# Kernel tuning notes

Hardware: AMD Instinct MI355X
Metric: run time of the kernel (lower is better)

The kernel has to match this reference:

```python
import jax, jax.numpy as jnp
import numpy as np

TOP_K = 2
EPS = 1e-6

def setup_inputs() -> dict:
    key = jax.random.key(0)
    ks = jax.random.split(key, 6)
    Bt, S, D, E, R = 4, 4096, 1024, 8, 4
    s = lambda d: 1.0 / np.sqrt(d)
    return {
        "x": jax.random.normal(ks[0], (Bt, S, D), jnp.float32),
        "W_base": jax.random.normal(ks[1], (D, D), jnp.float32) * s(D),
        "b_base": jax.random.normal(ks[2], (D,), jnp.float32) * 0.02,
        "W_router": jax.random.normal(ks[3], (E, D), jnp.float32) * s(D),
        "A": jax.random.normal(ks[4], (E, D, R), jnp.float32) * s(D),
        "B": jax.random.normal(ks[5], (E, R, D), jnp.float32) * s(R),
    }

def reference(x, W_base, b_base, W_router, A, B):
    # frozen base linear: [b,s,d] @ [out,d]^T + bias
    base_out = jnp.einsum('bsd,od->bso', x, W_base) + b_base
    # router softmax gate over experts
    logits = jnp.einsum('bsd,ed->bse', x, W_router)
    gate = jax.nn.softmax(logits, axis=-1)
    # top-k scatter-mask (values kept are the gate values themselves)
    topv, topi = jax.lax.top_k(gate, TOP_K)                    # [b,s,k]
    mask = jnp.sum(jax.nn.one_hot(topi, gate.shape[-1], dtype=gate.dtype), axis=-2)
    gate = gate * mask
    gate = gate / (jnp.sum(gate, axis=-1, keepdims=True) + EPS)
    # batched rank-4 LoRA experts, gating applied in low-rank space
    h = jnp.einsum('bsd,edr->bser', x, A)                      # [b,s,E,r]
    hg = h * gate[..., None]                                   # weight before up-proj
    lora_out = jnp.einsum('bser,ero->bso', hg, B)
    return base_out + lora_out
```

## Files before the change

kernel.cpp:

```cpp
#include <hip/hip_runtime.h>
#include <cstdint>

typedef __attribute__((ext_vector_type(8))) short short8;
typedef __attribute__((ext_vector_type(4))) float f32x4;

__device__ inline unsigned short f2bf(float f){
  union { float f; uint32_t u; } v; v.f = f;
  uint32_t r = v.u + 0x7FFFu + ((v.u >> 16) & 1u);
  return (unsigned short)(r >> 16);
}

#define GLL(gp, lp) __builtin_amdgcn_global_load_lds(              \
    (const __attribute__((address_space(1))) void*)(gp),           \
    (__attribute__((address_space(3))) void*)(lp), 16, 0, 0)

__global__ __launch_bounds__(256) void kconv(const float* __restrict__ W,
                                             const float* __restrict__ A,
                                             const float* __restrict__ Bm,
                                             unsigned short* __restrict__ Wb,
                                             unsigned short* __restrict__ BTt,
                                             unsigned short* __restrict__ W2b){
  int i = blockIdx.x * 256 + threadIdx.x;
  Wb[i] = f2bf(W[i]);
  if (i < 32768){
    int o = i >> 5, c = i & 31;
    BTt[i] = f2bf(Bm[(size_t)c*1024 + o]);
    int n = i >> 10, d = i & 1023;
    W2b[i] = f2bf(A[(((size_t)(n>>2))*1024 + d)*4 + (n&3)]);
  }
}

__global__ __launch_bounds__(256) void kxl(const float* __restrict__ x,
                                           const float* __restrict__ Wr,
                                           unsigned short* __restrict__ xb,
                                           float* __restrict__ gate){
  __shared__ float wr[8192];
  const int tid  = threadIdx.x;
  const int lane = tid & 63;
  const int w    = tid >> 6;
  {
    const float4* s  = (const float4*)Wr;
    float4*       d4 = (float4*)wr;
    #pragma unroll
    for (int j=0;j<8;j++) d4[j*256+tid] = s[j*256+tid];
  }
  __syncthreads();
  const float4* wr4 = (const float4*)wr;
  #pragma unroll 1
  for (int tt=0; tt<4; tt++){
    const size_t tok = (size_t)blockIdx.x*16 + w*4 + tt;
    const float4* xr = (const float4*)(x + tok*1024);
    ushort4*      xd = (ushort4*)(xb + tok*1024);
    float4 xv[4];
    #pragma unroll
    for (int c=0;c<4;c++){
      xv[c] = xr[c*64 + lane];
      ushort4 o4; o4.x=f2bf(xv[c].x); o4.y=f2bf(xv[c].y);
      o4.z=f2bf(xv[c].z); o4.w=f2bf(xv[c].w);
      xd[c*64 + lane] = o4;
    }
    float p[8];
    #pragma unroll
    for (int e=0;e<8;e++){
      float a = 0.f;
      #pragma unroll
      for (int c=0;c<4;c++){
        float4 wv = wr4[e*256 + c*64 + lane];
        a += xv[c].x*wv.x + xv[c].y*wv.y + xv[c].z*wv.z + xv[c].w*wv.w;
      }
      p[e] = a;
    }
    #pragma unroll
    for (int off=32; off; off>>=1){
      #pragma unroll
      for (int e=0;e<8;e++) p[e] += __shfl_xor(p[e], off, 64);
    }
    if (lane == 0){
      float mx = p[0];
      #pragma unroll
      for (int e=1;e<8;e++) mx = fmaxf(mx, p[e]);
      float ex[8], s2 = 0.f;
      #pragma unroll
      for (int e=0;e<8;e++){ ex[e] = __expf(p[e]-mx); s2 += ex[e]; }
      int i1 = 0; float v1 = ex[0];
      #pragma unroll
      for (int e=1;e<8;e++) if (ex[e] > v1){ v1 = ex[e]; i1 = e; }
      int i2 = -1; float v2 = -1.f;
      #pragma unroll
      for (int e=0;e<8;e++) if (e != i1 && ex[e] > v2){ v2 = ex[e]; i2 = e; }
      float g1 = v1/s2, g2 = v2/s2;
      float rs = 1.f/(g1 + g2 + 1e-6f);
      float* go = gate + tok*8;
      #pragma unroll
      for (int e=0;e<8;e++) go[e] = (e==i1 ? g1 : (e==i2 ? g2 : 0.f)) * rs;
    }
  }
}

__global__ __launch_bounds__(256) void kh(const unsigned short* __restrict__ xbp,
                                          const unsigned short* __restrict__ W2b,
                                          const float* __restrict__ gate,
                                          unsigned short* __restrict__ HG){
  const int tid  = threadIdx.x;
  const int lane = tid & 63;
  const int wid  = tid >> 6;
  const int lrow = lane & 15;
  const int lk   = (lane >> 4) * 8;
  const int tok0 = blockIdx.x*64 + wid*16;
  f32x4 acc0 = {0.f,0.f,0.f,0.f}, acc1 = {0.f,0.f,0.f,0.f};
  const unsigned short* b0 = W2b + (size_t)lrow*1024 + lk;
  const unsigned short* b1 = W2b + (size_t)(16+lrow)*1024 + lk;
  const unsigned short* ar = xbp + (size_t)(tok0+lrow)*1024 + lk;
  #pragma unroll 4
  for (int ks=0; ks<32; ks++){
    short8 av  = *(const short8*)(ar + ks*32);
    short8 bv0 = *(const short8*)(b0 + ks*32);
    short8 bv1 = *(const short8*)(b1 + ks*32);
    acc0 = __builtin_amdgcn_mfma_f32_16x16x32_bf16(av, bv0, acc0, 0, 0, 0);
    acc1 = __builtin_amdgcn_mfma_f32_16x16x32_bf16(av, bv1, acc1, 0, 0, 0);
  }
  #pragma unroll
  for (int j=0;j<4;j++){
    int tok = tok0 + (lane>>4)*4 + j;
    float g0 = gate[(size_t)tok*8 + (lrow>>2)];
    float g1 = gate[(size_t)tok*8 + 4 + (lrow>>2)];
    HG[(size_t)tok*32 + lrow]      = f2bf(acc0[j]*g0);
    HG[(size_t)tok*32 + 16 + lrow] = f2bf(acc1[j]*g1);
  }
}

__global__ __launch_bounds__(512, 2) void kgemm3(const unsigned short* __restrict__ xb,
                                                 const unsigned short* __restrict__ Wb,
                                                 const unsigned short* __restrict__ BTt,
                                                 const unsigned short* __restrict__ HG,
                                                 const float* __restrict__ bias,
                                                 float* __restrict__ out){
  __shared__ char lds[131072];
  char* ldsc = lds;
  const int tid  = threadIdx.x;
  const int lane = tid & 63;
  const int w    = tid >> 6;
  const int xcd  = blockIdx.x & 7, jj = blockIdx.x >> 3;
  const int nblk = xcd >> 1;
  const int mblk = (xcd & 1)*32 + jj;
  const int m0 = mblk << 8, n0 = nblk << 8;
  const int wm = w >> 2, wn = w & 3;
  const int lrow = lane & 15;
  const int q    = lane >> 4;

  const int swzk = (lrow & 7) << 4;
  int offA[8], offB[4];
  #pragma unroll
  for (int fm=0; fm<8; fm++){ int r = wm*128 + fm*16 + lrow; offA[fm] = r*128 + ((q<<4) ^ swzk); }
  #pragma unroll
  for (int fn=0; fn<4; fn++){ int r = wn*64  + fn*16 + lrow; offB[fn] = r*128 + ((q<<4) ^ swzk); }

  const int rowL = lane >> 3;
  const int colb = ((lane & 7) ^ rowL) << 4;
  const int rbA = (w>>2)*128 + (w&3)*16;
  const int rbB = w*16;
  const char* AgA = (const char*)xb + ((size_t)(m0 + rbA + rowL) << 11) + colb;
  const char* BgA = (const char*)Wb + ((size_t)(n0 + rbB + rowL) << 11) + colb;

#define STG_A(tt, h, ss) do{                                                        \
    GLL(AgA + (size_t)(h)*131072 + (tt)*128,                                        \
        ldsc + (ss)*32768 + (rbA + (h)*64)*128 + lane*16);                          \
    GLL(AgA + (size_t)(h)*131072 + 16384 + (tt)*128,                                \
        ldsc + (ss)*32768 + (rbA + (h)*64 + 8)*128 + lane*16); }while(0)
#define STG_B(tt, h, ss) do{                                                        \
    GLL(BgA + (size_t)(h)*262144 + (tt)*128,                                        \
        ldsc + 65536 + (ss)*32768 + (rbB + (h)*128)*128 + lane*16);                 \
    GLL(BgA + (size_t)(h)*262144 + 16384 + (tt)*128,                                \
        ldsc + 65536 + (ss)*32768 + (rbB + (h)*128 + 8)*128 + lane*16); }while(0)

  f32x4 acc[8][4];
  #pragma unroll
  for (int a=0;a<8;a++)
    #pragma unroll
    for (int b=0;b<4;b++) acc[a][b] = (f32x4){0.f,0.f,0.f,0.f};

  STG_A(0,0,0); STG_A(0,1,0); STG_B(0,0,0); STG_B(0,1,0);
  STG_A(1,0,1); STG_A(1,1,1);
  asm volatile("s_waitcnt vmcnt(4)" ::: "memory");
  __builtin_amdgcn_s_barrier();

  #pragma unroll 1
  for (int t = 0; t < 16; ++t){
    const int s = t & 1, sn = s ^ 1;
    const char* Ab = ldsc + s*32768;
    const char* Bb = ldsc + 65536 + s*32768;
    short8 a[8], b0[4], b1[4];
    #pragma unroll
    for (int fm=0; fm<4; fm++){
      a[fm*2]   = *(const short8*)(Ab + offA[fm]);
      a[fm*2+1] = *(const short8*)(Ab + (offA[fm]^64));
    }
    #pragma unroll
    for (int fn=0; fn<2; fn++){
      b0[fn*2]   = *(const short8*)(Bb + offB[fn]);
      b0[fn*2+1] = *(const short8*)(Bb + (offB[fn]^64));
    }
    if (t < 15) STG_B(t+1, 0, sn);
    __builtin_amdgcn_s_barrier();
    __builtin_amdgcn_s_setprio(1);
    #pragma unroll
    for (int kk=0;kk<2;kk++)
      #pragma unroll
      for (int fm=0;fm<4;fm++)
        #pragma unroll
        for (int fn=0;fn<2;fn++)
          acc[fm][fn] = __builtin_amdgcn_mfma_f32_16x16x32_bf16(a[fm*2+kk], b0[fn*2+kk], acc[fm][fn], 0, 0, 0);
    __builtin_amdgcn_s_setprio(0);
    __builtin_amdgcn_s_barrier();
    #pragma unroll
    for (int fn=0; fn<2; fn++){
      b1[fn*2]   = *(const short8*)(Bb + offB[2+fn]);
      b1[fn*2+1] = *(const short8*)(Bb + (offB[2+fn]^64));
    }
    if (t < 15) STG_B(t+1, 1, sn);
    __builtin_amdgcn_s_barrier();
    __builtin_amdgcn_s_setprio(1);
    #pragma unroll
    for (int kk=0;kk<2;kk++)
      #pragma unroll
      for (int fm=0;fm<4;fm++)
        #pragma unroll
        for (int fn=0;fn<2;fn++)
          acc[fm][2+fn] = __builtin_amdgcn_mfma_f32_16x16x32_bf16(a[fm*2+kk], b1[fn*2+kk], acc[fm][2+fn], 0, 0, 0);
    __builtin_amdgcn_s_setprio(0);
    __builtin_amdgcn_s_barrier();
    #pragma unroll
    for (int fm=0; fm<4; fm++){
      a[fm*2]   = *(const short8*)(Ab + offA[4+fm]);
      a[fm*2+1] = *(const short8*)(Ab + (offA[4+fm]^64));
    }
    if (t < 14) STG_A(t+2, 0, s);
    __builtin_amdgcn_s_barrier();
    __builtin_amdgcn_s_setprio(1);
    #pragma unroll
    for (int kk=0;kk<2;kk++)
      #pragma unroll
      for (int fm=0;fm<4;fm++)
        #pragma unroll
        for (int fn=0;fn<2;fn++)
          acc[4+fm][2+fn] = __builtin_amdgcn_mfma_f32_16x16x32_bf16(a[fm*2+kk], b1[fn*2+kk], acc[4+fm][2+fn], 0, 0, 0);
    __builtin_amdgcn_s_setprio(0);
    __builtin_amdgcn_s_barrier();
    if (t < 14){
      STG_A(t+2, 1, s);
      asm volatile("s_waitcnt vmcnt(4)" ::: "memory");
    } else {
      asm volatile("s_waitcnt vmcnt(0)" ::: "memory");
    }
    __builtin_amdgcn_s_barrier();
    __builtin_amdgcn_s_setprio(1);
    #pragma unroll
    for (int kk=0;kk<2;kk++)
      #pragma unroll
      for (int fm=0;fm<4;fm++)
        #pragma unroll
        for (int fn=0;fn<2;fn++)
          acc[4+fm][fn] = __builtin_amdgcn_mfma_f32_16x16x32_bf16(a[fm*2+kk], b0[fn*2+kk], acc[4+fm][fn], 0, 0, 0);
    __builtin_amdgcn_s_setprio(0);
    __builtin_amdgcn_s_barrier();
  }

  {
    const int colb2 = (((lane & 3) ^ ((lane >> 3) & 3)) << 4);
    const char* Hg = (const char*)HG  + (size_t)(m0 + w*32 + (lane>>2))*64 + colb2;
    const char* Tg = (const char*)BTt + (size_t)(n0 + w*32 + (lane>>2))*64 + colb2;
    const int dst2 = w*2048 + lane*16;
    GLL(Hg,        ldsc + dst2);
    GLL(Hg + 1024, ldsc + dst2 + 1024);
    GLL(Tg,        ldsc + 65536 + dst2);
    GLL(Tg + 1024, ldsc + 65536 + dst2 + 1024);
    asm volatile("s_waitcnt vmcnt(0)" ::: "memory");
    __builtin_amdgcn_s_barrier();
    const int swz2 = ((lrow >> 1) & 3) << 4;
    short8 hb[4];
    #pragma unroll
    for (int fn=0; fn<4; fn++){
      int r = wn*64 + fn*16 + lrow;
      hb[fn] = *(const short8*)(ldsc + 65536 + r*64 + ((q<<4) ^ swz2));
    }
    #pragma unroll
    for (int fm=0; fm<8; fm++){
      int r = wm*128 + fm*16 + lrow;
      short8 ha = *(const short8*)(ldsc + r*64 + ((q<<4) ^ swz2));
      #pragma unroll
      for (int fn=0; fn<4; fn++)
        acc[fm][fn] = __builtin_amdgcn_mfma_f32_16x16x32_bf16(ha, hb[fn], acc[fm][fn], 0, 0, 0);
    }
  }

  #pragma unroll
  for (int fn=0;fn<4;fn++){
    int col = n0 + wn*64 + fn*16 + lrow;
    float bv = bias[col];
    #pragma unroll
    for (int fm=0;fm<8;fm++){
      int rb = m0 + wm*128 + fm*16 + q*4;
      #pragma unroll
      for (int j=0;j<4;j++)
        out[(size_t)(rb+j)*1024 + col] = acc[fm][fn][j] + bv;
    }
  }
#undef STG_A
#undef STG_B
}

extern "C" void kernel_launch(void* const* d_in, const int* in_sizes, int n_in,
                              void* d_out, int out_size, void* d_ws, size_t ws_size,
                              hipStream_t stream){
  const float* x  = (const float*)d_in[0];
  const float* W  = (const float*)d_in[1];
  const float* bb = (const float*)d_in[2];
  const float* Wr = (const float*)d_in[3];
  const float* A  = (const float*)d_in[4];
  const float* Bm = (const float*)d_in[5];
  float* out = (float*)d_out;
  char* ws = (char*)d_ws;

  unsigned short* Wb   = (unsigned short*)(ws + 0);
  unsigned short* BTt  = (unsigned short*)(ws + 2097152);
  unsigned short* W2b  = (unsigned short*)(ws + 2162688);
  float*          gate = (float*)         (ws + 2228224);
  unsigned short* HG   = (unsigned short*)(ws + 2752512);
  unsigned short* xb   = (unsigned short*)(ws + 3801088);

  kconv<<<4096, 256, 0, stream>>>(W, A, Bm, Wb, BTt, W2b);
  kxl<<<1024, 256, 0, stream>>>(x, Wr, xb, gate);
  kh<<<256, 256, 0, stream>>>(xb, W2b, gate, HG);
  kgemm3<<<256, 512, 0, stream>>>(xb, Wb, BTt, HG, bb, out);
}
```

Measured before the change: 95.85 us.

## Restage GEMM prefetch schedule with inline-asm LDS reads and retile router kernel

The router/cast kernel now assigns 8 lanes per token (32 tokens per block) and accumulates across the row with a 3-step shuffle reduction, instead of one wave per token with a full 64-lane reduction, halving the grid. The main GEMM changes its global-to-LDS staging order: A and B for tile t+1 are issued progressively across the four MFMA phases into the other buffer, with explicit vmcnt waits. LDS fragment reads are done via inline ds_read_b128 with explicit lgkmcnt waits and sched_barriers to control instruction ordering. This aims to smooth memory issue and reduce reduction overhead, at the risk of less prefetch distance (one tile instead of two for A) and tighter wait-count correctness.

```diff
diff --git a/kernel.cpp b/kernel.cpp
--- a/kernel.cpp
+++ b/kernel.cpp
@@ -13,6 +13,8 @@
 #define GLL(gp, lp) __builtin_amdgcn_global_load_lds(              \
     (const __attribute__((address_space(1))) void*)(gp),           \
     (__attribute__((address_space(3))) void*)(lp), 16, 0, 0)
+
+#define DSR(dst, addr) asm volatile("ds_read_b128 %0, %1" : "=v"(dst) : "v"(addr))
 
 __global__ __launch_bounds__(256) void kconv(const float* __restrict__ W,
                                              const float* __restrict__ A,
@@ -30,14 +32,14 @@
   }
 }
 
-__global__ __launch_bounds__(256) void kxl(const float* __restrict__ x,
-                                           const float* __restrict__ Wr,
-                                           unsigned short* __restrict__ xb,
-                                           float* __restrict__ gate){
+__global__ __launch_bounds__(256) void kxl2(const float* __restrict__ x,
+                                            const float* __restrict__ Wr,
+                                            unsigned short* __restrict__ xb,
+                                            float* __restrict__ gate){
   __shared__ float wr[8192];
   const int tid  = threadIdx.x;
   const int lane = tid & 63;
-  const int w    = tid >> 6;
+  const int wid  = tid >> 6;
   {
     const float4* s  = (const float4*)Wr;
     float4*       d4 = (float4*)wr;
@@ -45,55 +47,46 @@
     for (int j=0;j<8;j++) d4[j*256+tid] = s[j*256+tid];
   }
   __syncthreads();
-  const float4* wr4 = (const float4*)wr;
-  #pragma unroll 1
-  for (int tt=0; tt<4; tt++){
-    const size_t tok = (size_t)blockIdx.x*16 + w*4 + tt;
-    const float4* xr = (const float4*)(x + tok*1024);
-    ushort4*      xd = (ushort4*)(xb + tok*1024);
-    float4 xv[4];
-    #pragma unroll
-    for (int c=0;c<4;c++){
-      xv[c] = xr[c*64 + lane];
-      ushort4 o4; o4.x=f2bf(xv[c].x); o4.y=f2bf(xv[c].y);
-      o4.z=f2bf(xv[c].z); o4.w=f2bf(xv[c].w);
-      xd[c*64 + lane] = o4;
+  const int tk  = lane >> 3, ln8 = lane & 7;
+  const size_t tok = (size_t)blockIdx.x*32 + wid*8 + tk;
+  const float4* xr = (const float4*)(x + tok*1024);
+  ushort4*      xd = (ushort4*)(xb + tok*1024);
+  const float4* wv = (const float4*)wr;
+  float p[8] = {0.f,0.f,0.f,0.f,0.f,0.f,0.f,0.f};
+  #pragma unroll 4
+  for (int it=0; it<32; it++){
+    float4 v = xr[it*8 + ln8];
+    ushort4 o; o.x=f2bf(v.x); o.y=f2bf(v.y); o.z=f2bf(v.z); o.w=f2bf(v.w);
+    xd[it*8 + ln8] = o;
+    #pragma unroll
+    for (int e=0;e<8;e++){
+      float4 wq = wv[e*256 + it*8 + ln8];
+      p[e] += v.x*wq.x + v.y*wq.y + v.z*wq.z + v.w*wq.w;
     }
-    float p[8];
-    #pragma unroll
-    for (int e=0;e<8;e++){
-      float a = 0.f;
-      #pragma unroll
-      for (int c=0;c<4;c++){
-        float4 wv = wr4[e*256 + c*64 + lane];
-        a += xv[c].x*wv.x + xv[c].y*wv.y + xv[c].z*wv.z + xv[c].w*wv.w;
-      }
-      p[e] = a;
-    }
-    #pragma unroll
-    for (int off=32; off; off>>=1){
-      #pragma unroll
-      for (int e=0;e<8;e++) p[e] += __shfl_xor(p[e], off, 64);
-    }
-    if (lane == 0){
-      float mx = p[0];
-      #pragma unroll
-      for (int e=1;e<8;e++) mx = fmaxf(mx, p[e]);
-      float ex[8], s2 = 0.f;
-      #pragma unroll
-      for (int e=0;e<8;e++){ ex[e] = __expf(p[e]-mx); s2 += ex[e]; }
-      int i1 = 0; float v1 = ex[0];
-      #pragma unroll
-      for (int e=1;e<8;e++) if (ex[e] > v1){ v1 = ex[e]; i1 = e; }
-      int i2 = -1; float v2 = -1.f;
-      #pragma unroll
-      for (int e=0;e<8;e++) if (e != i1 && ex[e] > v2){ v2 = ex[e]; i2 = e; }
-      float g1 = v1/s2, g2 = v2/s2;
-      float rs = 1.f/(g1 + g2 + 1e-6f);
-      float* go = gate + tok*8;
-      #pragma unroll
-      for (int e=0;e<8;e++) go[e] = (e==i1 ? g1 : (e==i2 ? g2 : 0.f)) * rs;
-    }
+  }
+  #pragma unroll
+  for (int off=1; off<8; off<<=1){
+    #pragma unroll
+    for (int e=0;e<8;e++) p[e] += __shfl_xor(p[e], off, 64);
+  }
+  if (ln8 == 0){
+    float mx = p[0];
+    #pragma unroll
+    for (int e=1;e<8;e++) mx = fmaxf(mx, p[e]);
+    float ex[8], s2 = 0.f;
+    #pragma unroll
+    for (int e=0;e<8;e++){ ex[e] = __expf(p[e]-mx); s2 += ex[e]; }
+    int i1 = 0; float v1 = ex[0];
+    #pragma unroll
+    for (int e=1;e<8;e++) if (ex[e] > v1){ v1 = ex[e]; i1 = e; }
+    int i2 = -1; float v2 = -1.f;
+    #pragma unroll
+    for (int e=0;e<8;e++) if (e != i1 && ex[e] > v2){ v2 = ex[e]; i2 = e; }
+    float g1 = v1/s2, g2 = v2/s2;
+    float rs = 1.f/(g1 + g2 + 1e-6f);
+    float* go = gate + tok*8;
+    #pragma unroll
+    for (int e=0;e<8;e++) go[e] = (e==i1 ? g1 : (e==i2 ? g2 : 0.f)) * rs;
   }
 }
 
@@ -129,14 +122,15 @@
   }
 }
 
-__global__ __launch_bounds__(512, 2) void kgemm3(const unsigned short* __restrict__ xb,
+__global__ __launch_bounds__(512, 2) void kgemm5(const unsigned short* __restrict__ xb,
                                                  const unsigned short* __restrict__ Wb,
                                                  const unsigned short* __restrict__ BTt,
                                                  const unsigned short* __restrict__ HG,
                                                  const float* __restrict__ bias,
                                                  float* __restrict__ out){
-  __shared__ char lds[131072];
+  __shared__ __attribute__((aligned(128))) char lds[131072];
   char* ldsc = lds;
+  const uint32_t L = (uint32_t)(uintptr_t)lds;
   const int tid  = threadIdx.x;
   const int lane = tid & 63;
   const int w    = tid >> 6;
@@ -149,7 +143,7 @@
   const int q    = lane >> 4;
 
   const int swzk = (lrow & 7) << 4;
-  int offA[8], offB[4];
+  uint32_t offA[8], offB[4];
   #pragma unroll
   for (int fm=0; fm<8; fm++){ int r = wm*128 + fm*16 + lrow; offA[fm] = r*128 + ((q<<4) ^ swzk); }
   #pragma unroll
@@ -158,50 +152,46 @@
   const int rowL = lane >> 3;
   const int colb = ((lane & 7) ^ rowL) << 4;
   const int rbA = (w>>2)*128 + (w&3)*16;
-  const int rbB = w*16;
-  const char* AgA = (const char*)xb + ((size_t)(m0 + rbA + rowL) << 11) + colb;
-  const char* BgA = (const char*)Wb + ((size_t)(n0 + rbB + rowL) << 11) + colb;
-
-#define STG_A(tt, h, ss) do{                                                        \
-    GLL(AgA + (size_t)(h)*131072 + (tt)*128,                                        \
-        ldsc + (ss)*32768 + (rbA + (h)*64)*128 + lane*16);                          \
-    GLL(AgA + (size_t)(h)*131072 + 16384 + (tt)*128,                                \
+  const int rbB = (w>>1)*64 + (w&1)*16;
+  const char* Ag = (const char*)xb + ((size_t)(m0 + rbA + rowL) << 11) + colb;
+  const char* Bg = (const char*)Wb + ((size_t)(n0 + rbB + rowL) << 11) + colb;
+
+#define STG_A(tt, h, ss) do{                                                    \
+    GLL(Ag + (size_t)(h)*131072 + (tt)*128,                                     \
+        ldsc + (ss)*32768 + (rbA + (h)*64)*128 + lane*16);                      \
+    GLL(Ag + (size_t)(h)*131072 + 16384 + (tt)*128,                             \
         ldsc + (ss)*32768 + (rbA + (h)*64 + 8)*128 + lane*16); }while(0)
-#define STG_B(tt, h, ss) do{                                                        \
-    GLL(BgA + (size_t)(h)*262144 + (tt)*128,                                        \
-        ldsc + 65536 + (ss)*32768 + (rbB + (h)*128)*128 + lane*16);                 \
-    GLL(BgA + (size_t)(h)*262144 + 16384 + (tt)*128,                                \
-        ldsc + 65536 + (ss)*32768 + (rbB + (h)*128 + 8)*128 + lane*16); }while(0)
+#define STG_B(tt, h, ss) do{                                                    \
+    GLL(Bg + (size_t)(h)*65536 + (tt)*128,                                      \
+        ldsc + 65536 + (ss)*32768 + (rbB + (h)*32)*128 + lane*16);              \
+    GLL(Bg + (size_t)(h)*65536 + 16384 + (tt)*128,                              \
+        ldsc + 65536 + (ss)*32768 + (rbB + (h)*32 + 8)*128 + lane*16); }while(0)
 
   f32x4 acc[8][4];
   #pragma unroll
-  for (int a=0;a<8;a++)
-    #pragma unroll
-    for (int b=0;b<4;b++) acc[a][b] = (f32x4){0.f,0.f,0.f,0.f};
+  for (int a2=0;a2<8;a2++)
+    #pragma unroll
+    for (int b2=0;b2<4;b2++) acc[a2][b2] = (f32x4){0.f,0.f,0.f,0.f};
 
   STG_A(0,0,0); STG_A(0,1,0); STG_B(0,0,0); STG_B(0,1,0);
-  STG_A(1,0,1); STG_A(1,1,1);
-  asm volatile("s_waitcnt vmcnt(4)" ::: "memory");
+  asm volatile("s_waitcnt vmcnt(0)" ::: "memory");
   __builtin_amdgcn_s_barrier();
 
+  short8 a[8], b0[4], b1[4];
   #pragma unroll 1
   for (int t = 0; t < 16; ++t){
     const int s = t & 1, sn = s ^ 1;
-    const char* Ab = ldsc + s*32768;
-    const char* Bb = ldsc + 65536 + s*32768;
-    short8 a[8], b0[4], b1[4];
-    #pragma unroll
-    for (int fm=0; fm<4; fm++){
-      a[fm*2]   = *(const short8*)(Ab + offA[fm]);
-      a[fm*2+1] = *(const short8*)(Ab + (offA[fm]^64));
-    }
-    #pragma unroll
-    for (int fn=0; fn<2; fn++){
-      b0[fn*2]   = *(const short8*)(Bb + offB[fn]);
-      b0[fn*2+1] = *(const short8*)(Bb + (offB[fn]^64));
-    }
-    if (t < 15) STG_B(t+1, 0, sn);
-    __builtin_amdgcn_s_barrier();
+    const uint32_t bA = L + s*32768;
+    const uint32_t bB = L + 65536 + s*32768;
+    #pragma unroll
+    for (int fm=0; fm<4; fm++){ DSR(a[fm*2], bA+offA[fm]); DSR(a[fm*2+1], bA+(offA[fm]^64u)); }
+    #pragma unroll
+    for (int fn=0; fn<2; fn++){ DSR(b0[fn*2], bB+offB[fn]); DSR(b0[fn*2+1], bB+(offB[fn]^64u)); }
+    if (t < 15){ STG_A(t+1, 0, sn); asm volatile("s_waitcnt vmcnt(2)" ::: "memory"); }
+    else       {                    asm volatile("s_waitcnt vmcnt(0)" ::: "memory"); }
+    __builtin_amdgcn_s_barrier();
+    asm volatile("s_waitcnt lgkmcnt(0)" ::: "memory");
+    __builtin_amdgcn_sched_barrier(0);
     __builtin_amdgcn_s_setprio(1);
     #pragma unroll
     for (int kk=0;kk<2;kk++)
@@ -213,12 +203,11 @@
     __builtin_amdgcn_s_setprio(0);
     __builtin_amdgcn_s_barrier();
     #pragma unroll
-    for (int fn=0; fn<2; fn++){
-      b1[fn*2]   = *(const short8*)(Bb + offB[2+fn]);
-      b1[fn*2+1] = *(const short8*)(Bb + (offB[2+fn]^64));
-    }
-    if (t < 15) STG_B(t+1, 1, sn);
-    __builtin_amdgcn_s_barrier();
+    for (int fn=0; fn<2; fn++){ DSR(b1[fn*2], bB+offB[2+fn]); DSR(b1[fn*2+1], bB+(offB[2+fn]^64u)); }
+    if (t < 15) STG_A(t+1, 1, sn);
+    __builtin_amdgcn_s_barrier();
+    asm volatile("s_waitcnt lgkmcnt(0)" ::: "memory");
+    __builtin_amdgcn_sched_barrier(0);
     __builtin_amdgcn_s_setprio(1);
     #pragma unroll
     for (int kk=0;kk<2;kk++)
@@ -230,12 +219,11 @@
     __builtin_amdgcn_s_setprio(0);
     __builtin_amdgcn_s_barrier();
     #pragma unroll
-    for (int fm=0; fm<4; fm++){
-      a[fm*2]   = *(const short8*)(Ab + offA[4+fm]);
-      a[fm*2+1] = *(const short8*)(Ab + (offA[4+fm]^64));
-    }
-    if (t < 14) STG_A(t+2, 0, s);
-    __builtin_amdgcn_s_barrier();
+    for (int fm=0; fm<4; fm++){ DSR(a[fm*2], bA+offA[4+fm]); DSR(a[fm*2+1], bA+(offA[4+fm]^64u)); }
+    if (t < 15) STG_B(t+1, 0, sn);
+    __builtin_amdgcn_s_barrier();
+    asm volatile("s_waitcnt lgkmcnt(0)" ::: "memory");
+    __builtin_amdgcn_sched_barrier(0);
     __builtin_amdgcn_s_setprio(1);
     #pragma unroll
     for (int kk=0;kk<2;kk++)
@@ -246,12 +234,7 @@
           acc[4+fm][2+fn] = __builtin_amdgcn_mfma_f32_16x16x32_bf16(a[fm*2+kk], b1[fn*2+kk], acc[4+fm][2+fn], 0, 0, 0);
     __builtin_amdgcn_s_setprio(0);
     __builtin_amdgcn_s_barrier();
-    if (t < 14){
-      STG_A(t+2, 1, s);
-      asm volatile("s_waitcnt vmcnt(4)" ::: "memory");
-    } else {
-      asm volatile("s_waitcnt vmcnt(0)" ::: "memory");
-    }
+    if (t < 15){ STG_B(t+1, 1, sn); asm volatile("s_waitcnt vmcnt(2)" ::: "memory"); }
     __builtin_amdgcn_s_barrier();
     __builtin_amdgcn_s_setprio(1);
     #pragma unroll
@@ -329,7 +312,7 @@
   unsigned short* xb   = (unsigned short*)(ws + 3801088);
 
   kconv<<<4096, 256, 0, stream>>>(W, A, Bm, Wb, BTt, W2b);
-  kxl<<<1024, 256, 0, stream>>>(x, Wr, xb, gate);
+  kxl2<<<512, 256, 0, stream>>>(x, Wr, xb, gate);
   kh<<<256, 256, 0, stream>>>(xb, W2b, gate, HG);
-  kgemm3<<<256, 512, 0, stream>>>(xb, Wb, BTt, HG, bb, out);
-}
+  kgemm5<<<256, 512, 0, stream>>>(xb, Wb, BTt, HG, bb, out);
+}
```

After: 91.21 us. 1.05x faster.
